# Kernel tuning notes

Measured on AMD Instinct MI355X. Metric: run time of the kernel, lower is better.

The kernel has to match this reference:

```python
import jax, jax.numpy as jnp
import numpy as np

N = 50000      # nodes
E = 800000     # edges (avg degree 16)
D = 64         # num_node_features
H = 64         # hidden_channels
G = 512        # graphs in batch
OUT = 32       # final linear output
NEG_SLOPE = 0.2


def setup_inputs() -> dict:
    key = jax.random.key(0)
    ks = jax.random.split(key, 20)
    s = 0.1  # param init scale
    inp = {
        "x": jax.random.normal(ks[0], (N, D), jnp.float32),
        "edge_index": jax.random.randint(ks[1], (2, E), 0, N, dtype=jnp.int64),
        "batch": jnp.sort(jax.random.randint(ks[2], (N,), 0, G, dtype=jnp.int64)),
        # GATv2 layer 1 (D -> H)
        "Wl1": jax.random.normal(ks[3], (D, H), jnp.float32) * s,
        "bl1": jnp.zeros((H,), jnp.float32),
        "Wr1": jax.random.normal(ks[4], (D, H), jnp.float32) * s,
        "br1": jnp.zeros((H,), jnp.float32),
        "att1": jax.random.normal(ks[5], (H,), jnp.float32) * s,
        "bias1": jnp.zeros((H,), jnp.float32),
        # GATv2 layer 2 (H -> H)
        "Wl2": jax.random.normal(ks[6], (H, H), jnp.float32) * s,
        "bl2": jnp.zeros((H,), jnp.float32),
        "Wr2": jax.random.normal(ks[7], (H, H), jnp.float32) * s,
        "br2": jnp.zeros((H,), jnp.float32),
        "att2": jax.random.normal(ks[8], (H,), jnp.float32) * s,
        "bias2": jnp.zeros((H,), jnp.float32),
        # final classifier
        "lin_w": jax.random.normal(ks[9], (H, OUT), jnp.float32) * s,
        "lin_b": jnp.zeros((OUT,), jnp.float32),
    }
    return inp


def _gatv2(x, src, dst, Wl, bl, Wr, br, att, bias):
    # GATv2Conv, heads=1, PyG semantics: messages flow src -> dst
    xl = x @ Wl + bl                       # [N, H] source transform (also the message)
    xr = x @ Wr + br                       # [N, H] destination transform
    z = xl[src] + xr[dst]                  # [E, H] gather
    e = jax.nn.leaky_relu(z, NEG_SLOPE) @ att  # [E] edge scores
    # segment softmax over edges grouped by destination node
    m = jax.ops.segment_max(e, dst, num_segments=N)   # [N]
    ex = jnp.exp(e - m[dst])                          # [E]
    denom = jax.ops.segment_sum(ex, dst, num_segments=N)  # [N]
    alpha = ex / denom[dst]                            # [E]
    out = jax.ops.segment_sum(alpha[:, None] * xl[src], dst, num_segments=N)  # [N, H]
    return out + bias


def reference(x, edge_index, batch,
              Wl1, bl1, Wr1, br1, att1, bias1,
              Wl2, bl2, Wr2, br2, att2, bias2,
              lin_w, lin_b):
    src, dst = edge_index[0], edge_index[1]
    h = jax.nn.relu(_gatv2(x, src, dst, Wl1, bl1, Wr1, br1, att1, bias1))
    h = jax.nn.relu(_gatv2(h, src, dst, Wl2, bl2, Wr2, br2, att2, bias2))
    # global mean pool over graphs
    sums = jax.ops.segment_sum(h, batch, num_segments=G)          # [G, H]
    cnts = jax.ops.segment_sum(jnp.ones((h.shape[0],), h.dtype), batch, num_segments=G)
    pooled = sums / jnp.maximum(cnts, 1.0)[:, None]
    # dropout(p=0.5) is identity at inference
    return pooled @ lin_w + lin_b                                  # [G, 32]
```

## Files before the change

kernel.cpp:

```cpp
#include <hip/hip_runtime.h>
#include <hip/hip_fp16.h>
#include <math.h>


#define ELLC    48
#define OVF_CAP 65536
#define ECHUNK  2048

typedef int      vint4 __attribute__((ext_vector_type(4)));
typedef _Float16 half4 __attribute__((ext_vector_type(4)));
typedef float    f32x4 __attribute__((ext_vector_type(4)));

#define GROWS 32
template <typename T>
__device__ __forceinline__ void dual_gemm_slim(
    int bid, int t,
    const T* __restrict__ X,
    const float* __restrict__ Wl, const float* __restrict__ bl,
    const float* __restrict__ Wr, const float* __restrict__ br,
    _Float16* __restrict__ xl, float* __restrict__ xr, int n,
    float* xS) {
    int row0 = bid * GROWS;
    for (int i = t; i < GROWS * 16; i += 256) {
        int r = row0 + (i >> 4);
        f32x4 v;
        v[0] = 0.f; v[1] = 0.f; v[2] = 0.f; v[3] = 0.f;
        if (r < n) {
            if constexpr (sizeof(T) == 2) {
                half4 hv = __builtin_nontemporal_load(
                    &((const half4*)(X + (size_t)r * 64))[i & 15]);
                v[0] = (float)hv[0]; v[1] = (float)hv[1];
                v[2] = (float)hv[2]; v[3] = (float)hv[3];
            } else {
                v = __builtin_nontemporal_load(
                    &((const f32x4*)(X + (size_t)r * 64))[i & 15]);
            }
        }
        ((f32x4*)xS)[i] = v;
    }
    __syncthreads();
    int h  = t & 63;
    int rb = t >> 6;
    float accl[8], accr[8];
#pragma unroll
    for (int i = 0; i < 8; ++i) { accl[i] = 0.f; accr[i] = 0.f; }
#pragma unroll 4
    for (int d = 0; d < 64; ++d) {
        float wl = Wl[d * 64 + h];
        float wr = Wr[d * 64 + h];
#pragma unroll
        for (int i = 0; i < 8; ++i) {
            float xv = xS[(rb + 4 * i) * 64 + d];
            accl[i] += xv * wl;
            accr[i] += xv * wr;
        }
    }
    float blv = bl[h], brv = br[h];
#pragma unroll
    for (int i = 0; i < 8; ++i) {
        int r = row0 + rb + 4 * i;
        if (r < n) {
            __builtin_nontemporal_store((_Float16)(accl[i] + blv),
                                        &xl[(size_t)r * 64 + h]);
            __builtin_nontemporal_store(accr[i] + brv,
                                        &xr[(size_t)r * 64 + h]);
        }
    }
}

__global__ __launch_bounds__(256) void dual_gemm64_f16_kernel(
    const _Float16* __restrict__ X,
    const float* __restrict__ Wl, const float* __restrict__ bl,
    const float* __restrict__ Wr, const float* __restrict__ br,
    _Float16* __restrict__ xl, float* __restrict__ xr, int n) {
    __shared__ float xS[GROWS * 64];
    dual_gemm_slim<_Float16>(blockIdx.x, threadIdx.x, X, Wl, bl, Wr, br,
                             xl, xr, n, xS);
}

__global__ __launch_bounds__(256) void fill_gemm_kernel(
    const int* __restrict__ src, const int* __restrict__ dst,
    int* __restrict__ cnt, unsigned short* __restrict__ ell,
    int* __restrict__ novf, int* __restrict__ ovf_dst, int* __restrict__ ovf_src,
    int E, int N, int psize, int fb, int ggrid,
    const float* __restrict__ X,
    const float* __restrict__ Wl, const float* __restrict__ bl,
    const float* __restrict__ Wr, const float* __restrict__ br,
    _Float16* __restrict__ xl, float* __restrict__ xr) {
    __shared__ float xS[GROWS * 64];
    int b = blockIdx.x;
    int q = b / 24, r = b % 24;
    if (r >= 16) {
        int vg = q * 8 + (r - 16);
        if (vg < ggrid)
            dual_gemm_slim<float>(vg, threadIdx.x, X, Wl, bl, Wr, br,
                                  xl, xr, N, xS);
        return;
    }
    int vb = q * 16 + r;
    if (vb >= fb) return;
    int t     = threadIdx.x;
    int chunk = vb >> 3;
    int p     = vb & 7;
    int d0    = p * psize;
    int d1    = min(N, d0 + psize);
    int e0    = chunk * ECHUNK;
    int e1    = min(E, e0 + ECHUNK);
    int nq    = (e1 - e0) >> 2;
    const vint4* dst4 = (const vint4*)(dst + e0);
    const vint4* src4 = (const vint4*)(src + e0);

    auto scatter4 = [&](vint4 dv, vint4 sv) {
#pragma unroll
        for (int k = 0; k < 4; ++k) {
            int d = dv[k];
            int s = sv[k];
            if (d >= d0 && d < d1) {
                int pos = atomicAdd(&cnt[d], 1);
                if (pos < ELLC) {
                    ell[d * ELLC + pos] = (unsigned short)s;
                } else {
                    int j = atomicAdd(novf, 1);
                    if (j < OVF_CAP) { ovf_dst[j] = d; ovf_src[j] = s; }
                }
            }
        }
    };

    if (nq == (ECHUNK >> 2)) {
        vint4 dvA = __builtin_nontemporal_load(&dst4[t]);
        vint4 svA = __builtin_nontemporal_load(&src4[t]);
        vint4 dvB = __builtin_nontemporal_load(&dst4[t + 256]);
        vint4 svB = __builtin_nontemporal_load(&src4[t + 256]);
        scatter4(dvA, svA);
        scatter4(dvB, svB);
    } else {
        for (int qq = t; qq < nq; qq += 256) {
            vint4 dv = __builtin_nontemporal_load(&dst4[qq]);
            vint4 sv = __builtin_nontemporal_load(&src4[qq]);
            scatter4(dv, sv);
        }
        for (int e = e0 + (nq << 2) + t; e < e1; e += 256) {
            int d = dst[e];
            if (d >= d0 && d < d1) {
                int pos = atomicAdd(&cnt[d], 1);
                int s   = src[e];
                if (pos < ELLC) {
                    ell[d * ELLC + pos] = (unsigned short)s;
                } else {
                    int j = atomicAdd(novf, 1);
                    if (j < OVF_CAP) { ovf_dst[j] = d; ovf_src[j] = s; }
                }
            }
        }
    }
}

__global__ __launch_bounds__(256) void gat_aggregate_kernel(
    const _Float16* __restrict__ xl, const float* __restrict__ xr,
    const int* __restrict__ cnt, const unsigned short* __restrict__ ell,
    const int* __restrict__ novf, const int* __restrict__ ovf_dst,
    const int* __restrict__ ovf_src,
    const float* __restrict__ att, const float* __restrict__ bias,
    _Float16* __restrict__ out, int n) {
    int wid  = (blockIdx.x * blockDim.x + threadIdx.x) >> 6;
    int lane = threadIdx.x & 63;
    if (wid >= n) return;
    int g = lane >> 4;
    int l = lane & 15;
    int d = wid;

    float4 att4 = ((const float4*)att)[l];
    float4 b4   = ((const float4*)bias)[l];
    int deg_d = cnt[d];
    int nd  = min(deg_d, ELLC);
    int beg = d * ELLC;

    float  s   = 0.f;
    float4 acc = make_float4(0.f, 0.f, 0.f, 0.f);

    if (deg_d > 0) {
        int myidx = 0;
        if (lane < ELLC)
            myidx = (int)__builtin_nontemporal_load(&ell[beg + lane]);
        int i_first = __shfl(myidx, 0);

        f32x4 xrt = __builtin_nontemporal_load(
            &((const f32x4*)(xr + (size_t)d * 64))[l]);
        float4 xr4 = make_float4(xrt[0], xrt[1], xrt[2], xrt[3]);

        int niter = (nd + 7) >> 3;

        half4 ph0[6], ph1[6];
#pragma unroll
        for (int k = 0; k < 6; ++k) {
            if (k < niter) {
                int  sa = k * 8 + g, sb = sa + 4;
                int  i0 = __shfl(myidx, sa); if (sa >= nd) i0 = i_first;
                int  i1 = __shfl(myidx, sb); if (sb >= nd) i1 = i_first;
                ph0[k] = ((const half4*)(xl + (size_t)i0 * 64))[l];
                ph1[k] = ((const half4*)(xl + (size_t)i1 * 64))[l];
            }
        }

#pragma unroll
        for (int k = 0; k < 6; ++k) {
            if (k < niter) {
                int  sa = k * 8 + g, sb = sa + 4;
                bool aa = sa < nd,   ab = sb < nd;
                half4 h0 = ph0[k];
                half4 h1 = ph1[k];
                float4 x0 = make_float4((float)h0[0], (float)h0[1], (float)h0[2], (float)h0[3]);
                float4 x1 = make_float4((float)h1[0], (float)h1[1], (float)h1[2], (float)h1[3]);
                float z, c0 = 0.f, c1 = 0.f;
                z = x0.x + xr4.x; c0 += ((z > 0.f) ? z : 0.2f * z) * att4.x;
                z = x0.y + xr4.y; c0 += ((z > 0.f) ? z : 0.2f * z) * att4.y;
                z = x0.z + xr4.z; c0 += ((z > 0.f) ? z : 0.2f * z) * att4.z;
                z = x0.w + xr4.w; c0 += ((z > 0.f) ? z : 0.2f * z) * att4.w;
                z = x1.x + xr4.x; c1 += ((z > 0.f) ? z : 0.2f * z) * att4.x;
                z = x1.y + xr4.y; c1 += ((z > 0.f) ? z : 0.2f * z) * att4.y;
                z = x1.z + xr4.z; c1 += ((z > 0.f) ? z : 0.2f * z) * att4.z;
                z = x1.w + xr4.w; c1 += ((z > 0.f) ? z : 0.2f * z) * att4.w;
#pragma unroll
                for (int sh = 8; sh >= 1; sh >>= 1) {
                    c0 += __shfl_xor(c0, sh);
                    c1 += __shfl_xor(c1, sh);
                }
                float w0 = aa ? __expf(fminf(c0, 30.f)) : 0.f;
                float w1 = ab ? __expf(fminf(c1, 30.f)) : 0.f;
                s += w0 + w1;
                acc.x += w0 * x0.x + w1 * x1.x;
                acc.y += w0 * x0.y + w1 * x1.y;
                acc.z += w0 * x0.z + w1 * x1.z;
                acc.w += w0 * x0.w + w1 * x1.w;
            }
        }
        if (deg_d > ELLC) {
            int no = min(*novf, OVF_CAP);
            for (int j = g; j < no; j += 4) {
                bool active = (ovf_dst[j] == d);
                int  i0     = active ? ovf_src[j] : i_first;
                half4 h0 = ((const half4*)(xl + (size_t)i0 * 64))[l];
                float4 x0 = make_float4((float)h0[0], (float)h0[1], (float)h0[2], (float)h0[3]);
                float z, c0 = 0.f;
                z = x0.x + xr4.x; c0 += ((z > 0.f) ? z : 0.2f * z) * att4.x;
                z = x0.y + xr4.y; c0 += ((z > 0.f) ? z : 0.2f * z) * att4.y;
                z = x0.z + xr4.z; c0 += ((z > 0.f) ? z : 0.2f * z) * att4.z;
                z = x0.w + xr4.w; c0 += ((z > 0.f) ? z : 0.2f * z) * att4.w;
#pragma unroll
                for (int sh = 8; sh >= 1; sh >>= 1) c0 += __shfl_xor(c0, sh);
                float w0 = active ? __expf(fminf(c0, 30.f)) : 0.f;
                s += w0;
                acc.x += w0 * x0.x;
                acc.y += w0 * x0.y;
                acc.z += w0 * x0.z;
                acc.w += w0 * x0.w;
            }
        }
#pragma unroll
        for (int mask = 16; mask <= 32; mask <<= 1) {
            s     += __shfl_xor(s, mask);
            acc.x += __shfl_xor(acc.x, mask);
            acc.y += __shfl_xor(acc.y, mask);
            acc.z += __shfl_xor(acc.z, mask);
            acc.w += __shfl_xor(acc.w, mask);
        }
    }
    if (g == 0) {
        float inv = (s > 0.f) ? (1.f / s) : 0.f;
        half4 hv;
        hv[0] = (_Float16)fmaxf(acc.x * inv + b4.x, 0.f);
        hv[1] = (_Float16)fmaxf(acc.y * inv + b4.y, 0.f);
        hv[2] = (_Float16)fmaxf(acc.z * inv + b4.z, 0.f);
        hv[3] = (_Float16)fmaxf(acc.w * inv + b4.w, 0.f);
        __builtin_nontemporal_store(hv, (half4*)(out + (size_t)d * 64) + l);
    }
}

__global__ __launch_bounds__(256) void pool_final_kernel(
    const _Float16* __restrict__ h, const int* __restrict__ batch,
    const float* __restrict__ lin_w, const float* __restrict__ lin_b,
    float* __restrict__ out, int N, int G) {
    int g = blockIdx.x;
    int t = threadIdx.x;
    auto lb = [&](int key) {
        int lo = 0, hi = N;
        while (lo < hi) {
            int mid = (lo + hi) >> 1;
            if (batch[mid] < key) lo = mid + 1; else hi = mid;
        }
        return lo;
    };
    int start = lb(g), end = lb(g + 1);

    __shared__ float part[4][64];
    __shared__ float pooled[64];
    int f = t & 63, w = t >> 6;
    float acc = 0.f;
    for (int i = start + w; i < end; i += 4)
        acc += (float)__builtin_nontemporal_load(&h[(size_t)i * 64 + f]);
    part[w][f] = acc;
    __syncthreads();
    if (t < 64) {
        float s = part[0][t] + part[1][t] + part[2][t] + part[3][t];
        pooled[t] = s / fmaxf((float)(end - start), 1.f);
    }
    __syncthreads();
    if (t < 32) {
        float a = 0.f;
#pragma unroll 8
        for (int hh = 0; hh < 64; ++hh) a += pooled[hh] * lin_w[hh * 32 + t];
        out[g * 32 + t] = a + lin_b[t];
    }
}

extern "C" void kernel_launch(void* const* d_in, const int* in_sizes, int n_in,
                              void* d_out, int out_size, void* d_ws, size_t ws_size,
                              hipStream_t stream) {
    const float* x     = (const float*)d_in[0];
    const int*   ei    = (const int*)d_in[1];
    const int*   batch = (const int*)d_in[2];
    const float* Wl1   = (const float*)d_in[3];
    const float* bl1   = (const float*)d_in[4];
    const float* Wr1   = (const float*)d_in[5];
    const float* br1   = (const float*)d_in[6];
    const float* att1  = (const float*)d_in[7];
    const float* bias1 = (const float*)d_in[8];
    const float* Wl2   = (const float*)d_in[9];
    const float* bl2   = (const float*)d_in[10];
    const float* Wr2   = (const float*)d_in[11];
    const float* br2   = (const float*)d_in[12];
    const float* att2  = (const float*)d_in[13];
    const float* bias2 = (const float*)d_in[14];
    const float* lin_w = (const float*)d_in[15];
    const float* lin_b = (const float*)d_in[16];
    float* out = (float*)d_out;

    const int N = in_sizes[0] / 64;
    const int E = in_sizes[1] / 2;
    const int G = out_size / 32;
    const int* src = ei;
    const int* dst = ei + E;

    char*  ws  = (char*)d_ws;
    size_t off = 0;
    auto alloc = [&](size_t bytes) -> void* {
        void* p = ws + off;
        off += bytes;
        off = (off + 255) & ~(size_t)255;
        return p;
    };
    _Float16* xl   = (_Float16*)alloc((size_t)N * 64 * sizeof(_Float16));
    float* xr      = (float*)alloc((size_t)N * 64 * sizeof(float));
    _Float16* h1   = (_Float16*)alloc((size_t)N * 64 * sizeof(_Float16));
    int*   cnt     = (int*)alloc((size_t)N * sizeof(int));
    int*   novf    = (int*)alloc(256);
    char*  zend    = ws + off;
    unsigned short* ell = (unsigned short*)alloc((size_t)N * ELLC * sizeof(unsigned short));
    int*   ovf_dst = (int*)alloc((size_t)OVF_CAP * sizeof(int));
    int*   ovf_src = (int*)alloc((size_t)OVF_CAP * sizeof(int));

    (void)hipMemsetAsync(cnt, 0, (size_t)(zend - (char*)cnt), stream);

    int ggrid  = (N + GROWS - 1) / GROWS;
    int agrid  = (N + 3) / 4;
    int nchunk = (E + ECHUNK - 1) / ECHUNK;
    int fb     = nchunk * 8;
    int psize  = (N + 7) / 8;
    int ngroups = max((fb + 15) / 16, (ggrid + 7) / 8);
    int igrid   = ngroups * 24;

    fill_gemm_kernel<<<igrid, 256, 0, stream>>>(
        src, dst, cnt, ell, novf, ovf_dst, ovf_src, E, N, psize, fb, ggrid,
        x, Wl1, bl1, Wr1, br1, xl, xr);

    gat_aggregate_kernel<<<agrid, 256, 0, stream>>>(
        xl, xr, cnt, ell, novf, ovf_dst, ovf_src, att1, bias1, h1, N);

    dual_gemm64_f16_kernel<<<ggrid, 256, 0, stream>>>(
        h1, Wl2, bl2, Wr2, br2, xl, xr, N);

    gat_aggregate_kernel<<<agrid, 256, 0, stream>>>(
        xl, xr, cnt, ell, novf, ovf_dst, ovf_src, att2, bias2, h1, N);

    pool_final_kernel<<<G, 256, 0, stream>>>(h1, batch, lin_w, lin_b, out, N, G);
}
```

Before: 252.9 us.

## Drop destination-range partitioning in ELL fill and batch atomics per thread

Result: slower. 262.7 us (+3.9%).

```diff
diff --git a/kernel.cpp b/kernel.cpp
--- a/kernel.cpp
+++ b/kernel.cpp
@@ -5,7 +5,7 @@
 
 #define ELLC    48
 #define OVF_CAP 65536
-#define ECHUNK  2048
+#define ECHUNK  4096
 
 typedef int      vint4 __attribute__((ext_vector_type(4)));
 typedef _Float16 half4 __attribute__((ext_vector_type(4)));
@@ -82,75 +82,85 @@
     const int* __restrict__ src, const int* __restrict__ dst,
     int* __restrict__ cnt, unsigned short* __restrict__ ell,
     int* __restrict__ novf, int* __restrict__ ovf_dst, int* __restrict__ ovf_src,
-    int E, int N, int psize, int fb, int ggrid,
+    int E, int N, int fb, int ggrid,
     const float* __restrict__ X,
     const float* __restrict__ Wl, const float* __restrict__ bl,
     const float* __restrict__ Wr, const float* __restrict__ br,
     _Float16* __restrict__ xl, float* __restrict__ xr) {
     __shared__ float xS[GROWS * 64];
     int b = blockIdx.x;
-    int q = b / 24, r = b % 24;
-    if (r >= 16) {
-        int vg = q * 8 + (r - 16);
+    int q = b / 9, r = b % 9;
+    if (r >= 1) {
+        int vg = q * 8 + (r - 1);
         if (vg < ggrid)
             dual_gemm_slim<float>(vg, threadIdx.x, X, Wl, bl, Wr, br,
                                   xl, xr, N, xS);
         return;
     }
-    int vb = q * 16 + r;
-    if (vb >= fb) return;
-    int t     = threadIdx.x;
-    int chunk = vb >> 3;
-    int p     = vb & 7;
-    int d0    = p * psize;
-    int d1    = min(N, d0 + psize);
-    int e0    = chunk * ECHUNK;
-    int e1    = min(E, e0 + ECHUNK);
-    int nq    = (e1 - e0) >> 2;
+    if (q >= fb) return;
+    int t  = threadIdx.x;
+    int e0 = q * ECHUNK;
+    int e1 = min(E, e0 + ECHUNK);
+    int nq = (e1 - e0) >> 2;
     const vint4* dst4 = (const vint4*)(dst + e0);
     const vint4* src4 = (const vint4*)(src + e0);
 
-    auto scatter4 = [&](vint4 dv, vint4 sv) {
-#pragma unroll
-        for (int k = 0; k < 4; ++k) {
-            int d = dv[k];
-            int s = sv[k];
-            if (d >= d0 && d < d1) {
-                int pos = atomicAdd(&cnt[d], 1);
-                if (pos < ELLC) {
-                    ell[d * ELLC + pos] = (unsigned short)s;
-                } else {
-                    int j = atomicAdd(novf, 1);
-                    if (j < OVF_CAP) { ovf_dst[j] = d; ovf_src[j] = s; }
-                }
-            }
-        }
-    };
-
     if (nq == (ECHUNK >> 2)) {
-        vint4 dvA = __builtin_nontemporal_load(&dst4[t]);
-        vint4 svA = __builtin_nontemporal_load(&src4[t]);
-        vint4 dvB = __builtin_nontemporal_load(&dst4[t + 256]);
-        vint4 svB = __builtin_nontemporal_load(&src4[t + 256]);
-        scatter4(dvA, svA);
-        scatter4(dvB, svB);
+        vint4 dv0 = __builtin_nontemporal_load(&dst4[t]);
+        vint4 dv1 = __builtin_nontemporal_load(&dst4[t + 256]);
+        vint4 dv2 = __builtin_nontemporal_load(&dst4[t + 512]);
+        vint4 dv3 = __builtin_nontemporal_load(&dst4[t + 768]);
+        vint4 sv0 = __builtin_nontemporal_load(&src4[t]);
+        vint4 sv1 = __builtin_nontemporal_load(&src4[t + 256]);
+        vint4 sv2 = __builtin_nontemporal_load(&src4[t + 512]);
+        vint4 sv3 = __builtin_nontemporal_load(&src4[t + 768]);
+        int d[16], s[16], p[16];
+#pragma unroll
+        for (int j = 0; j < 4; ++j) {
+            d[j]      = dv0[j]; s[j]      = sv0[j];
+            d[4 + j]  = dv1[j]; s[4 + j]  = sv1[j];
+            d[8 + j]  = dv2[j]; s[8 + j]  = sv2[j];
+            d[12 + j] = dv3[j]; s[12 + j] = sv3[j];
+        }
+#pragma unroll
+        for (int k = 0; k < 16; ++k) p[k] = atomicAdd(&cnt[d[k]], 1);
+#pragma unroll
+        for (int k = 0; k < 16; ++k) {
+            if (p[k] < ELLC) {
+                ell[d[k] * ELLC + p[k]] = (unsigned short)s[k];
+            } else {
+                int j = atomicAdd(novf, 1);
+                if (j < OVF_CAP) { ovf_dst[j] = d[k]; ovf_src[j] = s[k]; }
+            }
+        }
     } else {
         for (int qq = t; qq < nq; qq += 256) {
             vint4 dv = __builtin_nontemporal_load(&dst4[qq]);
             vint4 sv = __builtin_nontemporal_load(&src4[qq]);
-            scatter4(dv, sv);
-        }
-        for (int e = e0 + (nq << 2) + t; e < e1; e += 256) {
-            int d = dst[e];
-            if (d >= d0 && d < d1) {
-                int pos = atomicAdd(&cnt[d], 1);
-                int s   = src[e];
-                if (pos < ELLC) {
-                    ell[d * ELLC + pos] = (unsigned short)s;
+            int p0 = atomicAdd(&cnt[dv[0]], 1);
+            int p1 = atomicAdd(&cnt[dv[1]], 1);
+            int p2 = atomicAdd(&cnt[dv[2]], 1);
+            int p3 = atomicAdd(&cnt[dv[3]], 1);
+            int pp[4] = {p0, p1, p2, p3};
+#pragma unroll
+            for (int k = 0; k < 4; ++k) {
+                if (pp[k] < ELLC) {
+                    ell[dv[k] * ELLC + pp[k]] = (unsigned short)sv[k];
                 } else {
                     int j = atomicAdd(novf, 1);
-                    if (j < OVF_CAP) { ovf_dst[j] = d; ovf_src[j] = s; }
+                    if (j < OVF_CAP) { ovf_dst[j] = dv[k]; ovf_src[j] = sv[k]; }
                 }
+            }
+        }
+        for (int e = e0 + (nq << 2) + t; e < e1; e += 256) {
+            int dd = dst[e];
+            int pos = atomicAdd(&cnt[dd], 1);
+            int ss  = src[e];
+            if (pos < ELLC) {
+                ell[dd * ELLC + pos] = (unsigned short)ss;
+            } else {
+                int j = atomicAdd(novf, 1);
+                if (j < OVF_CAP) { ovf_dst[j] = dd; ovf_src[j] = ss; }
             }
         }
     }
@@ -365,13 +375,12 @@
     int ggrid  = (N + GROWS - 1) / GROWS;
     int agrid  = (N + 3) / 4;
     int nchunk = (E + ECHUNK - 1) / ECHUNK;
-    int fb     = nchunk * 8;
-    int psize  = (N + 7) / 8;
-    int ngroups = max((fb + 15) / 16, (ggrid + 7) / 8);
-    int igrid   = ngroups * 24;
+    int fb     = nchunk;
+    int ngroups = max(fb, (ggrid + 7) / 8);
+    int igrid   = ngroups * 9;
 
     fill_gemm_kernel<<<igrid, 256, 0, stream>>>(
-        src, dst, cnt, ell, novf, ovf_dst, ovf_src, E, N, psize, fb, ggrid,
+        src, dst, cnt, ell, novf, ovf_dst, ovf_src, E, N, fb, ggrid,
         x, Wl1, bl1, Wr1, br1, xl, xr);
 
     gat_aggregate_kernel<<<agrid, 256, 0, stream>>>(
```
